# Kernel optimization log

Hardware: AMD Instinct MI355X
Metric: run time of the kernel (lower is better)

Reference implementation:

```python
import jax, jax.numpy as jnp
import numpy as np

N = 50000   # nodes
E = 600000  # edges
D = 128     # emb_dim
L = 5       # num_layers
ATOM_DIMS = np.array([119, 4, 11, 13, 11, 7, 13, 2, 9]) + 5   # per-feature vocab (+5 as in source)
BOND_DIMS = np.array([7, 22, 2]) + 5
BL_CENTERS = np.arange(0.0, 2.0, 0.1, dtype=np.float32)   # 20 centers, gamma 10
PR_CENTERS = np.arange(0.0, 1.0, 0.05, dtype=np.float32)  # 20 centers, gamma 1
BL_GAMMA = 10.0
PR_GAMMA = 1.0
BN_EPS = 1e-5


def setup_inputs() -> dict:
    key = jax.random.key(0)
    ks = jax.random.split(key, 16)
    scale = 1.0 / np.sqrt(D)
    atom_off = jnp.asarray(np.concatenate([[0], np.cumsum(ATOM_DIMS)[:-1]]), jnp.int32)
    bond_off = jnp.asarray(np.concatenate([[0], np.cumsum(BOND_DIMS)[:-1]]), jnp.int32)
    return {
        "x": jax.random.randint(ks[0], (N, 9), 0, 7, dtype=jnp.int32),
        "edge_index": jax.random.randint(ks[1], (2, E), 0, N, dtype=jnp.int32),
        "edge_attr_int": jax.random.randint(ks[2], (E, 3), 0, 7, dtype=jnp.int32),
        "edge_attr_float": jax.random.uniform(ks[3], (E, 2), dtype=jnp.float32),
        "atom_off": atom_off,
        "bond_off": bond_off,
        "atom_emb": jax.random.normal(ks[4], (int(ATOM_DIMS.sum()), D), jnp.float32) * scale,
        "bond_emb": jax.random.normal(ks[5], (L, int(BOND_DIMS.sum()), D), jnp.float32) * scale,
        "W_bl": jax.random.normal(ks[6], (L, len(BL_CENTERS), D), jnp.float32) * scale,
        "b_bl": jnp.zeros((L, D), jnp.float32),
        "W_pr": jax.random.normal(ks[7], (L, len(PR_CENTERS), D), jnp.float32) * scale,
        "b_pr": jnp.zeros((L, D), jnp.float32),
        "mlp_W1": jax.random.normal(ks[8], (L, D, D), jnp.float32) * scale,
        "mlp_b1": jnp.zeros((L, D), jnp.float32),
        "bn1_g": jnp.ones((L, D), jnp.float32),
        "bn1_b": jnp.zeros((L, D), jnp.float32),
        "mlp_W2": jax.random.normal(ks[9], (L, D, D), jnp.float32) * scale,
        "mlp_b2": jnp.zeros((L, D), jnp.float32),
        "eps_gin": jnp.zeros((L,), jnp.float32),
        "bn_g": jnp.ones((L, D), jnp.float32),
        "bn_b": jnp.zeros((L, D), jnp.float32),
    }


def _bn(h, g, b):
    # BatchNorm1d, training-mode batch statistics over the node axis
    m = h.mean(0)
    v = h.var(0)
    return (h - m) * jax.lax.rsqrt(v + BN_EPS) * g + b


def _rbf(x, centers, gamma):
    # exp(-gamma * (x - c)^2): [E] -> [E, n_centers]
    return jnp.exp(-gamma * jnp.square(x[:, None] - centers[None, :]))


def reference(x, edge_index, edge_attr_int, edge_attr_float, atom_off, bond_off,
              atom_emb, bond_emb, W_bl, b_bl, W_pr, b_pr,
              mlp_W1, mlp_b1, bn1_g, bn1_b, mlp_W2, mlp_b2,
              eps_gin, bn_g, bn_b):
    # AtomEncoder: sum of 9 categorical embeddings (flat table + offsets)
    h = atom_emb[x + atom_off[None, :]].sum(1)  # [N, D]
    src, dst = edge_index[0], edge_index[1]
    bl = _rbf(edge_attr_float[:, 0], jnp.asarray(BL_CENTERS), BL_GAMMA)  # [E, 20]
    pr = _rbf(edge_attr_float[:, 1], jnp.asarray(PR_CENTERS), PR_GAMMA)  # [E, 20]
    for l in range(L):
        # per-layer edge embedding: BondEncoder + BondFloatRBF
        e = bond_emb[l][edge_attr_int + bond_off[None, :]].sum(1)
        e = e + bl @ W_bl[l] + b_bl[l] + pr @ W_pr[l] + b_pr[l]
        # GINConv (aggr='add'): mlp((1+eps)*x + sum_j relu(x_j + e_ij))
        msg = jax.nn.relu(h[src] + e)                       # [E, D]
        agg = jax.ops.segment_sum(msg, dst, num_segments=N)  # [N, D]
        z = (1.0 + eps_gin[l]) * h + agg
        z = z @ mlp_W1[l] + mlp_b1[l]
        z = jax.nn.relu(_bn(z, bn1_g[l], bn1_b[l]))
        z = z @ mlp_W2[l] + mlp_b2[l]
        # outer per-layer BatchNorm; ReLU except last layer (drop_ratio=0)
        z = _bn(z, bn_g[l], bn_b[l])
        if l < L - 1:
            z = jax.nn.relu(z)
        h = z
    return h  # JK='last'
```

## Files before the change

kernel.cpp:

```cpp
#include <hip/hip_runtime.h>
#include <hip/hip_bf16.h>

#define GN 50000
#define GE 600000
#define DD 128
#define TQ 2048
#define NBOND 2268
#define TROWS (2*(TQ+1) + NBOND)
#define SCB 49
#define NBANK 16
#define SSET (NBANK*256)
#define NB 782
#define LDK 136

typedef __attribute__((ext_vector_type(8))) short short8;
typedef __attribute__((ext_vector_type(4))) unsigned short ushort4v;
typedef __attribute__((ext_vector_type(4))) float floatx4;

__device__ __forceinline__ unsigned short f2b(float f) {
    __hip_bfloat16 h = __float2bfloat16(f);
    return __builtin_bit_cast(unsigned short, h);
}
__device__ __forceinline__ float b2f_lo(unsigned int u) { return __uint_as_float(u << 16); }
__device__ __forceinline__ float b2f_hi(unsigned int u) { return __uint_as_float(u & 0xffff0000u); }
__device__ __forceinline__ float bs2f(short s) {
    return __uint_as_float(((unsigned int)(unsigned short)s) << 16);
}

__global__ __launch_bounds__(256) void atom_kernel(
    const int* __restrict__ x, const int* __restrict__ atom_off,
    const float* __restrict__ atom_emb, unsigned short* __restrict__ h)
{
    int t = blockIdx.x * 256 + threadIdx.x;
    if (t >= GN * DD) return;
    int n = t >> 7, d = t & 127;
    float s = 0.f;
#pragma unroll
    for (int f = 0; f < 9; f++) {
        int idx = x[n * 9 + f] + atom_off[f];
        s += atom_emb[idx * DD + d];
    }
    h[t] = f2b(s);
}

__global__ __launch_bounds__(256) void hist_kernel(const int* __restrict__ ei, int* __restrict__ count)
{
    int e = blockIdx.x * 256 + threadIdx.x;
    if (e < GE) atomicAdd(&count[ei[GE + e]], 1);
}

__global__ __launch_bounds__(1024) void scan1_kernel(
    const int* __restrict__ count, int* __restrict__ row_start, int* __restrict__ blocksum)
{
    __shared__ int sh[1024];
    int t = threadIdx.x;
    int idx = blockIdx.x * 1024 + t;
    int v = (idx < GN) ? count[idx] : 0;
    sh[t] = v;
    __syncthreads();
    for (int off = 1; off < 1024; off <<= 1) {
        int u = (t >= off) ? sh[t - off] : 0;
        __syncthreads();
        sh[t] += u;
        __syncthreads();
    }
    if (idx <= GN) row_start[idx] = (t == 0) ? 0 : sh[t - 1];
    if (t == 1023) blocksum[blockIdx.x] = sh[1023];
}

__global__ __launch_bounds__(64) void scan2_kernel(
    const int* __restrict__ blocksum, int* __restrict__ blockoff)
{
    int t = threadIdx.x;
    int v = (t < SCB) ? blocksum[t] : 0;
#pragma unroll
    for (int off = 1; off < 64; off <<= 1) {
        int u = __shfl_up(v, off);
        if (t >= off) v += u;
    }
    int e = __shfl_up(v, 1);
    if (t == 0) e = 0;
    if (t < SCB) blockoff[t] = e;
}

__global__ __launch_bounds__(1024) void scan3_kernel(
    int* __restrict__ row_start, const int* __restrict__ blockoff)
{
    int idx = blockIdx.x * 1024 + threadIdx.x;
    if (idx <= GN) row_start[idx] += blockoff[blockIdx.x];
}

__global__ __launch_bounds__(256) void scatter_kernel(
    const int* __restrict__ ei, const int* __restrict__ eai, const float* __restrict__ eaf,
    const int* __restrict__ row_start, int* __restrict__ fill, int4* __restrict__ ep)
{
    int e = blockIdx.x * 256 + threadIdx.x;
    if (e < GE) {
        int d = ei[GE + e];
        int p = row_start[d] + atomicAdd(&fill[d], 1);
        int src = ei[e];
        float x1 = eaf[2 * e], x2 = eaf[2 * e + 1];
        int q1 = (int)(x1 * (float)TQ + 0.5f); q1 = min(max(q1, 0), TQ);
        int q2 = (int)(x2 * (float)TQ + 0.5f); q2 = min(max(q2, 0), TQ);
        int b0 = eai[3 * e], b1 = eai[3 * e + 1], b2 = eai[3 * e + 2];
        ep[p] = make_int4(src, q1 | (q2 << 16), (b0 * 27 + b1) * 7 + b2, 0);
    }
}

__global__ __launch_bounds__(128) void tables_kernel(
    const float* __restrict__ W_bl, const float* __restrict__ b_bl,
    const float* __restrict__ W_pr, const float* __restrict__ b_pr,
    const float* __restrict__ bond_emb, const int* __restrict__ bond_off,
    unsigned short* __restrict__ tbl_bl, unsigned short* __restrict__ tbl_pr,
    unsigned short* __restrict__ tbl_bond)
{
    int l = blockIdx.x / TROWS;
    int b = blockIdx.x % TROWS;
    int d = threadIdx.x;
    const float* W_bl_l = W_bl + (size_t)l * 20 * DD;
    const float* W_pr_l = W_pr + (size_t)l * 20 * DD;
    const float* bemb_l = bond_emb + (size_t)l * 46 * DD;
    if (b < (TQ + 1)) {
        float xq = b * (1.0f / TQ);
        float s = b_bl[(size_t)l * DD + d] + b_pr[(size_t)l * DD + d];
#pragma unroll
        for (int k = 0; k < 20; k++) {
            float dl = xq - 0.1f * k;
            s += __expf(-10.f * dl * dl) * W_bl_l[k * DD + d];
        }
        tbl_bl[((size_t)l * (TQ + 1) + b) * DD + d] = f2b(s);
    } else if (b < 2 * (TQ + 1)) {
        int q = b - (TQ + 1);
        float xq = q * (1.0f / TQ);
        float s = 0.f;
#pragma unroll
        for (int k = 0; k < 20; k++) {
            float dl = xq - 0.05f * k;
            s += __expf(-dl * dl) * W_pr_l[k * DD + d];
        }
        tbl_pr[((size_t)l * (TQ + 1) + q) * DD + d] = f2b(s);
    } else {
        int r = b - 2 * (TQ + 1);
        int b0 = r / 189;
        int rem = r % 189;
        int b1 = rem / 7, b2 = rem % 7;
        tbl_bond[((size_t)l * NBOND + r) * DD + d] =
            f2b(bemb_l[(b0 + bond_off[0]) * DD + d]
              + bemb_l[(b1 + bond_off[1]) * DD + d]
              + bemb_l[(b2 + bond_off[2]) * DD + d]);
    }
}

__global__ __launch_bounds__(256) void wfrag_kernel(
    const float* __restrict__ W1, const float* __restrict__ W2,
    unsigned short* __restrict__ wf_hi, unsigned short* __restrict__ wf_lo)
{
    int t = blockIdx.x * 256 + threadIdx.x;
    if (t >= 10 * 2048) return;
    int mat = t >> 11;
    int rem = t & 2047;
    int kt = rem >> 9;
    int rem2 = rem & 511;
    int nt = rem2 >> 6;
    int lane = rem2 & 63;
    const float* src = (mat & 1) ? (W2 + (size_t)(mat >> 1) * DD * DD)
                                 : (W1 + (size_t)(mat >> 1) * DD * DD);
    int n = nt * 16 + (lane & 15);
    int k0 = kt * 32 + (lane >> 4) * 8;
    size_t base = (size_t)mat * 16384 + (size_t)((kt * 8 + nt) * 64 + lane) * 8;
#pragma unroll
    for (int j = 0; j < 8; j++) {
        float w = src[(size_t)(k0 + j) * DD + n];
        unsigned short hi = f2b(w);
        wf_hi[base + j] = hi;
        wf_lo[base + j] = f2b(w - bs2f((short)hi));
    }
}

template <int BN>
__global__ __launch_bounds__(256) void edge_kernel(
    const int4* __restrict__ ep,
    const unsigned short* __restrict__ tbl_bl, const unsigned short* __restrict__ tbl_pr,
    const unsigned short* __restrict__ tbl_bond,
    const unsigned short* __restrict__ hsrc, const int* __restrict__ row_start,
    const float* __restrict__ eps_gin, int layer,
    const float* __restrict__ stats_prev, const float* __restrict__ g_prev,
    const float* __restrict__ b_prev,
    float* __restrict__ A)
{
    __shared__ float sc_s[DD], tr_s[DD];
    int tid = threadIdx.x;
    if (BN) {
        if (tid < DD) {
            float s = 0.f, q = 0.f;
#pragma unroll
            for (int bk = 0; bk < NBANK; bk++) {
                s += stats_prev[bk * 256 + tid];
                q += stats_prev[bk * 256 + 128 + tid];
            }
            float m = s * (1.0f / GN);
            float v = q * (1.0f / GN) - m * m;
            float sc = g_prev[tid] * rsqrtf(v + 1e-5f);
            sc_s[tid] = sc;
            tr_s[tid] = b_prev[tid] - m * sc;
        }
        __syncthreads();
    }

    int wid = __builtin_amdgcn_readfirstlane(tid >> 6);
    int lane = tid & 63;
    float sc0 = 1.f, tr0 = 0.f, sc1 = 1.f, tr1 = 0.f;
    if (BN) {
        sc0 = sc_s[2 * lane];     tr0 = tr_s[2 * lane];
        sc1 = sc_s[2 * lane + 1]; tr1 = tr_s[2 * lane + 1];
    }

    int n = blockIdx.x * 4 + wid;
    int s0 = __builtin_amdgcn_readfirstlane(row_start[n]);
    int s1 = __builtin_amdgcn_readfirstlane(row_start[n + 1]);
    const unsigned int* hu = (const unsigned int*)hsrc;
    const unsigned int* tb = (const unsigned int*)tbl_bl;
    const unsigned int* tp = (const unsigned int*)tbl_pr;
    const unsigned int* tg = (const unsigned int*)tbl_bond;
    float a0 = 0.f, a1 = 0.f;

    auto meta = [&](int pb, int4 (&mm)[4]) {
#pragma unroll
        for (int j = 0; j < 4; j++) mm[j] = ep[pb + j];
    };
    auto issue = [&](const int4 (&mm)[4], unsigned int (&ub)[4], unsigned int (&up)[4],
                     unsigned int (&ug)[4], unsigned int (&uh)[4]) {
#pragma unroll
        for (int j = 0; j < 4; j++) {
            ub[j] = tb[(size_t)(mm[j].y & 0xffff) * 64 + lane];
            up[j] = tp[(size_t)((unsigned)mm[j].y >> 16) * 64 + lane];
            ug[j] = tg[(size_t)mm[j].z * 64 + lane];
            uh[j] = hu[(size_t)mm[j].x * 64 + lane];
        }
    };
    auto consume = [&](const unsigned int (&ub)[4], const unsigned int (&up)[4],
                       const unsigned int (&ug)[4], const unsigned int (&uh)[4]) {
#pragma unroll
        for (int j = 0; j < 4; j++) {
            float h0, h1;
            if (BN) {
                h0 = fmaxf(fmaf(b2f_lo(uh[j]), sc0, tr0), 0.f);
                h1 = fmaxf(fmaf(b2f_hi(uh[j]), sc1, tr1), 0.f);
            } else {
                h0 = b2f_lo(uh[j]);
                h1 = b2f_hi(uh[j]);
            }
            a0 += fmaxf(h0 + b2f_lo(ub[j]) + b2f_lo(up[j]) + b2f_lo(ug[j]), 0.f);
            a1 += fmaxf(h1 + b2f_hi(ub[j]) + b2f_hi(up[j]) + b2f_hi(ug[j]), 0.f);
        }
    };

    int cnt = s1 - s0;
    int nfull = cnt >> 2;
    {
        int4 mA[4], mB[4];
        unsigned int ubA[4], upA[4], ugA[4], uhA[4];
        unsigned int ubB[4], upB[4], ugB[4], uhB[4];
        if (nfull > 0) {
            meta(s0, mA);
            issue(mA, ubA, upA, ugA, uhA);
            int i = 1;
            for (; i + 1 < nfull; i += 2) {
                meta(s0 + i * 4, mB);
                meta(s0 + (i + 1) * 4, mA);
                issue(mB, ubB, upB, ugB, uhB);
                consume(ubA, upA, ugA, uhA);
                issue(mA, ubA, upA, ugA, uhA);
                consume(ubB, upB, ugB, uhB);
            }
            if (i < nfull) {
                meta(s0 + i * 4, mB);
                issue(mB, ubB, upB, ugB, uhB);
                consume(ubA, upA, ugA, uhA);
                consume(ubB, upB, ugB, uhB);
            } else {
                consume(ubA, upA, ugA, uhA);
            }
        }
    }
    for (int p = s0 + nfull * 4; p < s1; p++) {
        int4 m0 = ep[p];
        unsigned int ub0 = tb[(size_t)(m0.y & 0xffff) * 64 + lane];
        unsigned int up0 = tp[(size_t)((unsigned)m0.y >> 16) * 64 + lane];
        unsigned int ug0 = tg[(size_t)m0.z * 64 + lane];
        unsigned int uh0 = hu[(size_t)m0.x * 64 + lane];
        float h00, h01;
        if (BN) {
            h00 = fmaxf(fmaf(b2f_lo(uh0), sc0, tr0), 0.f);
            h01 = fmaxf(fmaf(b2f_hi(uh0), sc1, tr1), 0.f);
        } else {
            h00 = b2f_lo(uh0);
            h01 = b2f_hi(uh0);
        }
        a0 += fmaxf(h00 + b2f_lo(ub0) + b2f_lo(up0) + b2f_lo(ug0), 0.f);
        a1 += fmaxf(h01 + b2f_hi(ub0) + b2f_hi(up0) + b2f_hi(ug0), 0.f);
    }

    float eps1 = 1.f + eps_gin[layer];
    unsigned int un = hu[(size_t)n * 64 + lane];
    float n0, n1;
    if (BN) {
        n0 = fmaxf(fmaf(b2f_lo(un), sc0, tr0), 0.f);
        n1 = fmaxf(fmaf(b2f_hi(un), sc1, tr1), 0.f);
    } else {
        n0 = b2f_lo(un);
        n1 = b2f_hi(un);
    }
    a0 += eps1 * n0;
    a1 += eps1 * n1;
    float2 o; o.x = a0; o.y = a1;
    *(float2*)(A + (size_t)n * DD + 2 * lane) = o;
}

template <int MODE>
__global__ __launch_bounds__(256) void gemm_kernel(
    const float* __restrict__ Asrc,
    const unsigned short* __restrict__ wf_hi, const unsigned short* __restrict__ wf_lo,
    const float* __restrict__ bias,
    unsigned short* __restrict__ Cbf, float* __restrict__ Cf32, int out_bf16,
    const float* __restrict__ stats_in, const float* __restrict__ bn_g,
    const float* __restrict__ bn_b, float* __restrict__ stats_out)
{
    __shared__ unsigned short Ahi[64 * LDK];
    __shared__ unsigned short Alo[64 * LDK];
    __shared__ float sc_s[DD], tr_s[DD];
    int tid = threadIdx.x, wid = tid >> 6, lane = tid & 63;
    int row0 = blockIdx.x * 64;

    if (MODE == 1) {
        if (tid < DD) {
            float s = 0.f, q = 0.f;
#pragma unroll
            for (int bk = 0; bk < NBANK; bk++) {
                s += stats_in[bk * 256 + tid];
                q += stats_in[bk * 256 + 128 + tid];
            }
            float m = s * (1.0f / GN);
            float v = q * (1.0f / GN) - m * m;
            float sc = bn_g[tid] * rsqrtf(v + 1e-5f);
            sc_s[tid] = sc;
            tr_s[tid] = bn_b[tid] - m * sc;
        }
        __syncthreads();
    }

    {
        const float* g = Asrc + (size_t)row0 * DD;
#pragma unroll
        for (int i = 0; i < 8; i++) {
            int idx = i * 1024 + tid * 4;
            float4 v = *(const float4*)(g + idx);
            int r = idx >> 7, c = idx & 127;
            if (MODE == 1) {
                v.x = fmaxf(v.x * sc_s[c]     + tr_s[c],     0.f);
                v.y = fmaxf(v.y * sc_s[c + 1] + tr_s[c + 1], 0.f);
                v.z = fmaxf(v.z * sc_s[c + 2] + tr_s[c + 2], 0.f);
                v.w = fmaxf(v.w * sc_s[c + 3] + tr_s[c + 3], 0.f);
            }
            ushort4v hi, lo;
            hi[0] = f2b(v.x); lo[0] = f2b(v.x - bs2f((short)hi[0]));
            hi[1] = f2b(v.y); lo[1] = f2b(v.y - bs2f((short)hi[1]));
            hi[2] = f2b(v.z); lo[2] = f2b(v.z - bs2f((short)hi[2]));
            hi[3] = f2b(v.w); lo[3] = f2b(v.w - bs2f((short)hi[3]));
            *(ushort4v*)(Ahi + r * LDK + c) = hi;
            *(ushort4v*)(Alo + r * LDK + c) = lo;
        }
    }
    __syncthreads();

    int quad = lane >> 4, l16 = lane & 15;
    floatx4 acc[4][2];
#pragma unroll
    for (int rt = 0; rt < 4; rt++)
#pragma unroll
        for (int nt = 0; nt < 2; nt++) acc[rt][nt] = (floatx4){0.f, 0.f, 0.f, 0.f};

    const short8* bhp = (const short8*)wf_hi;
    const short8* blp = (const short8*)wf_lo;
#pragma unroll
    for (int kt = 0; kt < 4; kt++) {
        short8 ahi[4], alo[4];
        int kb = kt * 32 + quad * 8;
#pragma unroll
        for (int rt = 0; rt < 4; rt++) {
            int ro = (rt * 16 + l16) * LDK + kb;
            ahi[rt] = *(const short8*)(Ahi + ro);
            alo[rt] = *(const short8*)(Alo + ro);
        }
#pragma unroll
        for (int nt = 0; nt < 2; nt++) {
            int ntg = wid * 2 + nt;
            short8 bhi = bhp[(kt * 8 + ntg) * 64 + lane];
            short8 blo = blp[(kt * 8 + ntg) * 64 + lane];
#pragma unroll
            for (int rt = 0; rt < 4; rt++) {
                acc[rt][nt] = __builtin_amdgcn_mfma_f32_16x16x32_bf16(ahi[rt], bhi, acc[rt][nt], 0, 0, 0);
                acc[rt][nt] = __builtin_amdgcn_mfma_f32_16x16x32_bf16(alo[rt], bhi, acc[rt][nt], 0, 0, 0);
                acc[rt][nt] = __builtin_amdgcn_mfma_f32_16x16x32_bf16(ahi[rt], blo, acc[rt][nt], 0, 0, 0);
            }
        }
    }

    int bank = blockIdx.x & (NBANK - 1);
#pragma unroll
    for (int nt = 0; nt < 2; nt++) {
        int col = (wid * 2 + nt) * 16 + l16;
        float bv = bias[col];
        float s = 0.f, q = 0.f;
#pragma unroll
        for (int rt = 0; rt < 4; rt++) {
#pragma unroll
            for (int v = 0; v < 4; v++) {
                int r = row0 + rt * 16 + quad * 4 + v;
                float o = acc[rt][nt][v] + bv;
                if (r < GN) {
                    s += o; q += o * o;
                    if (MODE == 1 && out_bf16) Cbf[(size_t)r * DD + col] = f2b(o);
                    else                       Cf32[(size_t)r * DD + col] = o;
                }
            }
        }
        s += __shfl_xor(s, 16); s += __shfl_xor(s, 32);
        q += __shfl_xor(q, 16); q += __shfl_xor(q, 32);
        if (lane < 16) {
            atomicAdd(&stats_out[bank * 256 + col], s);
            atomicAdd(&stats_out[bank * 256 + 128 + col], q);
        }
    }
}

__global__ __launch_bounds__(256) void bn_apply_kernel(
    const float* __restrict__ Z, const float* __restrict__ stats2,
    const float* __restrict__ g, const float* __restrict__ b,
    float* __restrict__ fout)
{
    __shared__ float sc_s[DD], tr_s[DD];
    int tid = threadIdx.x;
    if (tid < DD) {
        float s = 0.f, q = 0.f;
#pragma unroll
        for (int bk = 0; bk < NBANK; bk++) {
            s += stats2[bk * 256 + tid];
            q += stats2[bk * 256 + 128 + tid];
        }
        float m = s * (1.0f / GN);
        float v = q * (1.0f / GN) - m * m;
        float sc = g[tid] * rsqrtf(v + 1e-5f);
        sc_s[tid] = sc;
        tr_s[tid] = b[tid] - m * sc;
    }
    __syncthreads();
    const int total = GN * DD;
    for (int t = blockIdx.x * 256 + tid; t < total; t += gridDim.x * 256) {
        int c = t & 127;
        fout[t] = Z[t] * sc_s[c] + tr_s[c];
    }
}

extern "C" void kernel_launch(void* const* d_in, const int* in_sizes, int n_in,
                              void* d_out, int out_size, void* d_ws, size_t ws_size,
                              hipStream_t stream)
{
    const int*   x        = (const int*)d_in[0];
    const int*   ei       = (const int*)d_in[1];
    const int*   eai      = (const int*)d_in[2];
    const float* eaf      = (const float*)d_in[3];
    const int*   atom_off = (const int*)d_in[4];
    const int*   bond_off = (const int*)d_in[5];
    const float* atom_emb = (const float*)d_in[6];
    const float* bond_emb = (const float*)d_in[7];
    const float* W_bl     = (const float*)d_in[8];
    const float* b_bl     = (const float*)d_in[9];
    const float* W_pr     = (const float*)d_in[10];
    const float* b_pr     = (const float*)d_in[11];
    const float* W1       = (const float*)d_in[12];
    const float* b1       = (const float*)d_in[13];
    const float* bn1g     = (const float*)d_in[14];
    const float* bn1b     = (const float*)d_in[15];
    const float* W2       = (const float*)d_in[16];
    const float* b2       = (const float*)d_in[17];
    const float* eps_gin  = (const float*)d_in[18];
    const float* bng      = (const float*)d_in[19];
    const float* bnb      = (const float*)d_in[20];
    float* out = (float*)d_out;

    char* p = (char*)d_ws;
    unsigned short* h_bf  = (unsigned short*)p;  p += (size_t)GN * DD * 2;
    unsigned short* z2_bf = (unsigned short*)p;  p += (size_t)GN * DD * 2;
    float* A              = (float*)p;           p += (size_t)GN * DD * 4;
    float* z1             = (float*)p;           p += (size_t)GN * DD * 4;
    float* z2f            = (float*)p;           p += (size_t)GN * DD * 4;
    unsigned short* tbl_bl   = (unsigned short*)p;  p += (size_t)5 * (TQ + 1) * DD * 2;
    unsigned short* tbl_pr   = (unsigned short*)p;  p += (size_t)5 * (TQ + 1) * DD * 2;
    unsigned short* tbl_bond = (unsigned short*)p;  p += (size_t)5 * NBOND * DD * 2;
    unsigned short* wf_hi    = (unsigned short*)p;  p += (size_t)10 * 16384 * 2;
    unsigned short* wf_lo    = (unsigned short*)p;  p += (size_t)10 * 16384 * 2;
    float* stats_all = (float*)p;  p += (size_t)10 * SSET * 4;
    int* count    = (int*)p;    p += (size_t)GN * 4;
    int* fill     = (int*)p;    p += (size_t)GN * 4;
    int* row_start= (int*)p;    p += (size_t)(GN + 1) * 4;
    int* blocksum = (int*)p;    p += (size_t)SCB * 4;
    int* blockoff = (int*)p;    p += (size_t)SCB * 4;
    p = (char*)(((size_t)p + 15) & ~(size_t)15);
    int4* ep      = (int4*)p;   p += (size_t)GE * 16;

    hipMemsetAsync(count, 0, (size_t)GN * 4, stream);
    hipMemsetAsync(fill,  0, (size_t)GN * 4, stream);
    hipMemsetAsync(stats_all, 0, (size_t)10 * SSET * 4, stream);

    hist_kernel<<<(GE + 255) / 256, 256, 0, stream>>>(ei, count);
    scan1_kernel<<<SCB, 1024, 0, stream>>>(count, row_start, blocksum);
    scan2_kernel<<<1, 64, 0, stream>>>(blocksum, blockoff);
    scan3_kernel<<<SCB, 1024, 0, stream>>>(row_start, blockoff);
    scatter_kernel<<<(GE + 255) / 256, 256, 0, stream>>>(ei, eai, eaf, row_start, fill, ep);
    atom_kernel<<<(GN * DD + 255) / 256, 256, 0, stream>>>(x, atom_off, atom_emb, h_bf);
    wfrag_kernel<<<80, 256, 0, stream>>>(W1, W2, wf_hi, wf_lo);
    tables_kernel<<<5 * TROWS, 128, 0, stream>>>(
        W_bl, b_bl, W_pr, b_pr, bond_emb, bond_off, tbl_bl, tbl_pr, tbl_bond);

    for (int l = 0; l < 5; l++) {
        float* stats1 = stats_all + (size_t)(2 * l + 0) * SSET;
        float* stats2 = stats_all + (size_t)(2 * l + 1) * SSET;
        float* stats2_prev = stats_all + (size_t)(2 * (l - 1) + 1) * SSET;

        if (l == 0) {
            edge_kernel<0><<<GN / 4, 256, 0, stream>>>(
                ep, tbl_bl, tbl_pr, tbl_bond,
                h_bf, row_start, eps_gin, l,
                stats_all, bng, bnb, A);
        } else {
            edge_kernel<1><<<GN / 4, 256, 0, stream>>>(
                ep,
                tbl_bl + (size_t)l * (TQ + 1) * DD,
                tbl_pr + (size_t)l * (TQ + 1) * DD,
                tbl_bond + (size_t)l * NBOND * DD,
                z2_bf, row_start, eps_gin, l,
                stats2_prev,
                bng + (size_t)(l - 1) * DD,
                bnb + (size_t)(l - 1) * DD,
                A);
        }

        gemm_kernel<0><<<NB, 256, 0, stream>>>(
            A, wf_hi + (size_t)(l * 2 + 0) * 16384, wf_lo + (size_t)(l * 2 + 0) * 16384,
            b1 + (size_t)l * DD, nullptr, z1, 0,
            nullptr, nullptr, nullptr, stats1);

        gemm_kernel<1><<<NB, 256, 0, stream>>>(
            z1, wf_hi + (size_t)(l * 2 + 1) * 16384, wf_lo + (size_t)(l * 2 + 1) * 16384,
            b2 + (size_t)l * DD, z2_bf, z2f, (l < 4) ? 1 : 0,
            stats1, bn1g + (size_t)l * DD, bn1b + (size_t)l * DD, stats2);
    }

    bn_apply_kernel<<<1024, 256, 0, stream>>>(
        z2f, stats_all + (size_t)9 * SSET, bng + (size_t)4 * DD, bnb + (size_t)4 * DD, out);
}
```

Before: 646.0 us.

## Fuse edge aggregation with first MLP GEMM into one kernel

```diff
diff --git a/kernel.cpp b/kernel.cpp
--- a/kernel.cpp
+++ b/kernel.cpp
@@ -177,8 +177,8 @@
     }
 }
 
-template <int BN>
-__global__ __launch_bounds__(256) void edge_kernel(
+template <int L0>
+__global__ __launch_bounds__(512, 6) void eg1_kernel(
     const int4* __restrict__ ep,
     const unsigned short* __restrict__ tbl_bl, const unsigned short* __restrict__ tbl_pr,
     const unsigned short* __restrict__ tbl_bond,
@@ -186,11 +186,17 @@
     const float* __restrict__ eps_gin, int layer,
     const float* __restrict__ stats_prev, const float* __restrict__ g_prev,
     const float* __restrict__ b_prev,
-    float* __restrict__ A)
-{
+    const unsigned short* __restrict__ wf_hi, const unsigned short* __restrict__ wf_lo,
+    const float* __restrict__ bias,
+    float* __restrict__ z1, float* __restrict__ stats_out)
+{
+    __shared__ unsigned short Ahi[64 * LDK];
+    __shared__ unsigned short Alo[64 * LDK];
     __shared__ float sc_s[DD], tr_s[DD];
-    int tid = threadIdx.x;
-    if (BN) {
+    int tid = threadIdx.x, wid = tid >> 6, lane = tid & 63;
+    int row0 = blockIdx.x * 64;
+
+    if (!L0) {
         if (tid < DD) {
             float s = 0.f, q = 0.f;
 #pragma unroll
@@ -206,115 +212,172 @@
         }
         __syncthreads();
     }
-
-    int wid = __builtin_amdgcn_readfirstlane(tid >> 6);
-    int lane = tid & 63;
     float sc0 = 1.f, tr0 = 0.f, sc1 = 1.f, tr1 = 0.f;
-    if (BN) {
+    if (!L0) {
         sc0 = sc_s[2 * lane];     tr0 = tr_s[2 * lane];
         sc1 = sc_s[2 * lane + 1]; tr1 = tr_s[2 * lane + 1];
     }
 
-    int n = blockIdx.x * 4 + wid;
-    int s0 = __builtin_amdgcn_readfirstlane(row_start[n]);
-    int s1 = __builtin_amdgcn_readfirstlane(row_start[n + 1]);
-    const unsigned int* hu = (const unsigned int*)hsrc;
-    const unsigned int* tb = (const unsigned int*)tbl_bl;
-    const unsigned int* tp = (const unsigned int*)tbl_pr;
-    const unsigned int* tg = (const unsigned int*)tbl_bond;
-    float a0 = 0.f, a1 = 0.f;
-
-    auto meta = [&](int pb, int4 (&mm)[4]) {
-#pragma unroll
-        for (int j = 0; j < 4; j++) mm[j] = ep[pb + j];
-    };
-    auto issue = [&](const int4 (&mm)[4], unsigned int (&ub)[4], unsigned int (&up)[4],
-                     unsigned int (&ug)[4], unsigned int (&uh)[4]) {
-#pragma unroll
-        for (int j = 0; j < 4; j++) {
-            ub[j] = tb[(size_t)(mm[j].y & 0xffff) * 64 + lane];
-            up[j] = tp[(size_t)((unsigned)mm[j].y >> 16) * 64 + lane];
-            ug[j] = tg[(size_t)mm[j].z * 64 + lane];
-            uh[j] = hu[(size_t)mm[j].x * 64 + lane];
-        }
-    };
-    auto consume = [&](const unsigned int (&ub)[4], const unsigned int (&up)[4],
-                       const unsigned int (&ug)[4], const unsigned int (&uh)[4]) {
-#pragma unroll
-        for (int j = 0; j < 4; j++) {
-            float h0, h1;
-            if (BN) {
-                h0 = fmaxf(fmaf(b2f_lo(uh[j]), sc0, tr0), 0.f);
-                h1 = fmaxf(fmaf(b2f_hi(uh[j]), sc1, tr1), 0.f);
-            } else {
-                h0 = b2f_lo(uh[j]);
-                h1 = b2f_hi(uh[j]);
-            }
-            a0 += fmaxf(h0 + b2f_lo(ub[j]) + b2f_lo(up[j]) + b2f_lo(ug[j]), 0.f);
-            a1 += fmaxf(h1 + b2f_hi(ub[j]) + b2f_hi(up[j]) + b2f_hi(ug[j]), 0.f);
-        }
-    };
-
-    int cnt = s1 - s0;
-    int nfull = cnt >> 2;
     {
-        int4 mA[4], mB[4];
-        unsigned int ubA[4], upA[4], ugA[4], uhA[4];
-        unsigned int ubB[4], upB[4], ugB[4], uhB[4];
-        if (nfull > 0) {
-            meta(s0, mA);
-            issue(mA, ubA, upA, ugA, uhA);
-            int i = 1;
-            for (; i + 1 < nfull; i += 2) {
-                meta(s0 + i * 4, mB);
-                meta(s0 + (i + 1) * 4, mA);
-                issue(mB, ubB, upB, ugB, uhB);
-                consume(ubA, upA, ugA, uhA);
-                issue(mA, ubA, upA, ugA, uhA);
-                consume(ubB, upB, ugB, uhB);
-            }
-            if (i < nfull) {
-                meta(s0 + i * 4, mB);
-                issue(mB, ubB, upB, ugB, uhB);
-                consume(ubA, upA, ugA, uhA);
-                consume(ubB, upB, ugB, uhB);
-            } else {
-                consume(ubA, upA, ugA, uhA);
-            }
-        }
-    }
-    for (int p = s0 + nfull * 4; p < s1; p++) {
-        int4 m0 = ep[p];
-        unsigned int ub0 = tb[(size_t)(m0.y & 0xffff) * 64 + lane];
-        unsigned int up0 = tp[(size_t)((unsigned)m0.y >> 16) * 64 + lane];
-        unsigned int ug0 = tg[(size_t)m0.z * 64 + lane];
-        unsigned int uh0 = hu[(size_t)m0.x * 64 + lane];
-        float h00, h01;
-        if (BN) {
-            h00 = fmaxf(fmaf(b2f_lo(uh0), sc0, tr0), 0.f);
-            h01 = fmaxf(fmaf(b2f_hi(uh0), sc1, tr1), 0.f);
-        } else {
-            h00 = b2f_lo(uh0);
-            h01 = b2f_hi(uh0);
-        }
-        a0 += fmaxf(h00 + b2f_lo(ub0) + b2f_lo(up0) + b2f_lo(ug0), 0.f);
-        a1 += fmaxf(h01 + b2f_hi(ub0) + b2f_hi(up0) + b2f_hi(ug0), 0.f);
-    }
-
-    float eps1 = 1.f + eps_gin[layer];
-    unsigned int un = hu[(size_t)n * 64 + lane];
-    float n0, n1;
-    if (BN) {
-        n0 = fmaxf(fmaf(b2f_lo(un), sc0, tr0), 0.f);
-        n1 = fmaxf(fmaf(b2f_hi(un), sc1, tr1), 0.f);
-    } else {
-        n0 = b2f_lo(un);
-        n1 = b2f_hi(un);
-    }
-    a0 += eps1 * n0;
-    a1 += eps1 * n1;
-    float2 o; o.x = a0; o.y = a1;
-    *(float2*)(A + (size_t)n * DD + 2 * lane) = o;
+        const unsigned int* hu = (const unsigned int*)hsrc;
+        const unsigned int* tb = (const unsigned int*)tbl_bl;
+        const unsigned int* tp = (const unsigned int*)tbl_pr;
+        const unsigned int* tg = (const unsigned int*)tbl_bond;
+        float eps1 = 1.f + eps_gin[layer];
+        unsigned int* AhiW = (unsigned int*)Ahi;
+        unsigned int* AloW = (unsigned int*)Alo;
+
+        for (int i = 0; i < 8; i++) {
+            int lr = wid * 8 + i;
+            int n = row0 + lr;
+            float a0 = 0.f, a1 = 0.f;
+            if (n < GN) {
+                int s0 = __builtin_amdgcn_readfirstlane(row_start[n]);
+                int s1 = __builtin_amdgcn_readfirstlane(row_start[n + 1]);
+
+                auto meta = [&](int pb, int4 (&mm)[4]) {
+#pragma unroll
+                    for (int j = 0; j < 4; j++) mm[j] = ep[pb + j];
+                };
+                auto issue = [&](const int4 (&mm)[4], unsigned int (&ub)[4], unsigned int (&up)[4],
+                                 unsigned int (&ug)[4], unsigned int (&uh)[4]) {
+#pragma unroll
+                    for (int j = 0; j < 4; j++) {
+                        ub[j] = tb[(size_t)(mm[j].y & 0xffff) * 64 + lane];
+                        up[j] = tp[(size_t)((unsigned)mm[j].y >> 16) * 64 + lane];
+                        ug[j] = tg[(size_t)mm[j].z * 64 + lane];
+                        uh[j] = hu[(size_t)mm[j].x * 64 + lane];
+                    }
+                };
+                auto consume = [&](const unsigned int (&ub)[4], const unsigned int (&up)[4],
+                                   const unsigned int (&ug)[4], const unsigned int (&uh)[4]) {
+#pragma unroll
+                    for (int j = 0; j < 4; j++) {
+                        float h0, h1;
+                        if (!L0) {
+                            h0 = fmaxf(fmaf(b2f_lo(uh[j]), sc0, tr0), 0.f);
+                            h1 = fmaxf(fmaf(b2f_hi(uh[j]), sc1, tr1), 0.f);
+                        } else {
+                            h0 = b2f_lo(uh[j]);
+                            h1 = b2f_hi(uh[j]);
+                        }
+                        a0 += fmaxf(h0 + b2f_lo(ub[j]) + b2f_lo(up[j]) + b2f_lo(ug[j]), 0.f);
+                        a1 += fmaxf(h1 + b2f_hi(ub[j]) + b2f_hi(up[j]) + b2f_hi(ug[j]), 0.f);
+                    }
+                };
+
+                int nfull = (s1 - s0) >> 2;
+                {
+                    int4 mA[4], mB[4];
+                    unsigned int ubA[4], upA[4], ugA[4], uhA[4];
+                    unsigned int ubB[4], upB[4], ugB[4], uhB[4];
+                    if (nfull > 0) {
+                        meta(s0, mA);
+                        issue(mA, ubA, upA, ugA, uhA);
+                        int k = 1;
+                        for (; k + 1 < nfull; k += 2) {
+                            meta(s0 + k * 4, mB);
+                            meta(s0 + (k + 1) * 4, mA);
+                            issue(mB, ubB, upB, ugB, uhB);
+                            consume(ubA, upA, ugA, uhA);
+                            issue(mA, ubA, upA, ugA, uhA);
+                            consume(ubB, upB, ugB, uhB);
+                        }
+                        if (k < nfull) {
+                            meta(s0 + k * 4, mB);
+                            issue(mB, ubB, upB, ugB, uhB);
+                            consume(ubA, upA, ugA, uhA);
+                            consume(ubB, upB, ugB, uhB);
+                        } else {
+                            consume(ubA, upA, ugA, uhA);
+                        }
+                    }
+                }
+                for (int p = s0 + ((s1 - s0) >> 2) * 4; p < s1; p++) {
+                    int4 m0 = ep[p];
+                    unsigned int ub0 = tb[(size_t)(m0.y & 0xffff) * 64 + lane];
+                    unsigned int up0 = tp[(size_t)((unsigned)m0.y >> 16) * 64 + lane];
+                    unsigned int ug0 = tg[(size_t)m0.z * 64 + lane];
+                    unsigned int uh0 = hu[(size_t)m0.x * 64 + lane];
+                    float h00, h01;
+                    if (!L0) {
+                        h00 = fmaxf(fmaf(b2f_lo(uh0), sc0, tr0), 0.f);
+                        h01 = fmaxf(fmaf(b2f_hi(uh0), sc1, tr1), 0.f);
+                    } else {
+                        h00 = b2f_lo(uh0);
+                        h01 = b2f_hi(uh0);
+                    }
+                    a0 += fmaxf(h00 + b2f_lo(ub0) + b2f_lo(up0) + b2f_lo(ug0), 0.f);
+                    a1 += fmaxf(h01 + b2f_hi(ub0) + b2f_hi(up0) + b2f_hi(ug0), 0.f);
+                }
+
+                unsigned int un = hu[(size_t)n * 64 + lane];
+                float n0, n1;
+                if (!L0) {
+                    n0 = fmaxf(fmaf(b2f_lo(un), sc0, tr0), 0.f);
+                    n1 = fmaxf(fmaf(b2f_hi(un), sc1, tr1), 0.f);
+                } else {
+                    n0 = b2f_lo(un);
+                    n1 = b2f_hi(un);
+                }
+                a0 += eps1 * n0;
+                a1 += eps1 * n1;
+            }
+            unsigned short h0u = f2b(a0), h1u = f2b(a1);
+            AhiW[lr * (LDK / 2) + lane] = (unsigned int)h0u | ((unsigned int)h1u << 16);
+            unsigned short l0u = f2b(a0 - bs2f((short)h0u));
+            unsigned short l1u = f2b(a1 - bs2f((short)h1u));
+            AloW[lr * (LDK / 2) + lane] = (unsigned int)l0u | ((unsigned int)l1u << 16);
+        }
+    }
+    __syncthreads();
+
+    int quad = lane >> 4, l16 = lane & 15;
+    floatx4 acc[4];
+#pragma unroll
+    for (int rt = 0; rt < 4; rt++) acc[rt] = (floatx4){0.f, 0.f, 0.f, 0.f};
+    {
+        const short8* bhp = (const short8*)wf_hi;
+        const short8* blp = (const short8*)wf_lo;
+#pragma unroll
+        for (int kt = 0; kt < 4; kt++) {
+            int kb = kt * 32 + quad * 8;
+            short8 bhi = bhp[(kt * 8 + wid) * 64 + lane];
+            short8 blo = blp[(kt * 8 + wid) * 64 + lane];
+#pragma unroll
+            for (int rt = 0; rt < 4; rt++) {
+                int ro = (rt * 16 + l16) * LDK + kb;
+                short8 ahi = *(const short8*)(Ahi + ro);
+                short8 alo = *(const short8*)(Alo + ro);
+                acc[rt] = __builtin_amdgcn_mfma_f32_16x16x32_bf16(ahi, bhi, acc[rt], 0, 0, 0);
+                acc[rt] = __builtin_amdgcn_mfma_f32_16x16x32_bf16(alo, bhi, acc[rt], 0, 0, 0);
+                acc[rt] = __builtin_amdgcn_mfma_f32_16x16x32_bf16(ahi, blo, acc[rt], 0, 0, 0);
+            }
+        }
+    }
+
+    int bank = blockIdx.x & (NBANK - 1);
+    int col = wid * 16 + l16;
+    float bv = bias[col];
+    float s = 0.f, q = 0.f;
+#pragma unroll
+    for (int rt = 0; rt < 4; rt++) {
+#pragma unroll
+        for (int v = 0; v < 4; v++) {
+            int r = row0 + rt * 16 + quad * 4 + v;
+            float o = acc[rt][v] + bv;
+            if (r < GN) {
+                s += o; q += o * o;
+                z1[(size_t)r * DD + col] = o;
+            }
+        }
+    }
+    s += __shfl_xor(s, 16); s += __shfl_xor(s, 32);
+    q += __shfl_xor(q, 16); q += __shfl_xor(q, 32);
+    if (lane < 16) {
+        atomicAdd(&stats_out[bank * 256 + col], s);
+        atomicAdd(&stats_out[bank * 256 + 128 + col], q);
+    }
 }
 
 template <int MODE>
@@ -529,12 +592,14 @@
         float* stats2_prev = stats_all + (size_t)(2 * (l - 1) + 1) * SSET;
 
         if (l == 0) {
-            edge_kernel<0><<<GN / 4, 256, 0, stream>>>(
+            eg1_kernel<1><<<NB, 512, 0, stream>>>(
                 ep, tbl_bl, tbl_pr, tbl_bond,
                 h_bf, row_start, eps_gin, l,
-                stats_all, bng, bnb, A);
+                stats_all, bng, bnb,
+                wf_hi + (size_t)(l * 2 + 0) * 16384, wf_lo + (size_t)(l * 2 + 0) * 16384,
+                b1 + (size_t)l * DD, z1, stats1);
         } else {
-            edge_kernel<1><<<GN / 4, 256, 0, stream>>>(
+            eg1_kernel<0><<<NB, 512, 0, stream>>>(
                 ep,
                 tbl_bl + (size_t)l * (TQ + 1) * DD,
                 tbl_pr + (size_t)l * (TQ + 1) * DD,
@@ -543,13 +608,9 @@
                 stats2_prev,
                 bng + (size_t)(l - 1) * DD,
                 bnb + (size_t)(l - 1) * DD,
-                A);
-        }
-
-        gemm_kernel<0><<<NB, 256, 0, stream>>>(
-            A, wf_hi + (size_t)(l * 2 + 0) * 16384, wf_lo + (size_t)(l * 2 + 0) * 16384,
-            b1 + (size_t)l * DD, nullptr, z1, 0,
-            nullptr, nullptr, nullptr, stats1);
+                wf_hi + (size_t)(l * 2 + 0) * 16384, wf_lo + (size_t)(l * 2 + 0) * 16384,
+                b1 + (size_t)l * DD, z1, stats1);
+        }
 
         gemm_kernel<1><<<NB, 256, 0, stream>>>(
             z1, wf_hi + (size_t)(l * 2 + 1) * 16384, wf_lo + (size_t)(l * 2 + 1) * 16384,
```

Measured after the change: 688.4 us. 1.07x slower.
